# Optimization experiments

Hardware: AMD Instinct MI355X
Metric: run time of the kernel (lower is better)

Reference implementation:

```python
import jax, jax.numpy as jnp
import numpy as np

N_E = 16384
E_DIM = 256


def setup_inputs() -> dict:
    key = jax.random.key(0)
    k1, k2 = jax.random.split(key)
    z = jax.random.normal(k1, (16, E_DIM, 32, 32), dtype=jnp.float32)
    # nn.Embedding init: uniform(-1/n_e, 1/n_e)
    embedding_weight = jax.random.uniform(
        k2, (N_E, E_DIM), dtype=jnp.float32, minval=-1.0 / N_E, maxval=1.0 / N_E
    )
    return {"z": z, "embedding_weight": embedding_weight}


def reference(z, embedding_weight):
    # b c h w -> b h w c, flatten to (N, e_dim)
    zf = jnp.transpose(z, (0, 2, 3, 1)).reshape(-1, E_DIM)  # [N, d]
    # squared euclidean distances: ||z||^2 + ||e||^2 - 2 z.e^T
    d = (
        jnp.sum(zf ** 2, axis=1, keepdims=True)          # [N, 1]
        + jnp.sum(embedding_weight ** 2, axis=1)         # [n_e]
        - 2.0 * jnp.einsum("bd,nd->bn", zf, embedding_weight)  # [N, n_e]
    )
    min_encoding_indices = jnp.argmin(d, axis=1)  # [N] int
    return min_encoding_indices
```

## Files before the change

kernel.cpp:

```cpp
#include <hip/hip_runtime.h>

#define EDIM 256
#define NROW 16384
#define NCODE 16384
#define NBN 128
#define MARGIN 2.0e-4f

typedef _Float16 f16x8 __attribute__((ext_vector_type(8)));
typedef _Float16 f16x4 __attribute__((ext_vector_type(4)));
typedef float f32x4 __attribute__((ext_vector_type(4)));

__device__ __forceinline__ void gll16(const void* g, void* l) {
  __builtin_amdgcn_global_load_lds((const __attribute__((address_space(1))) void*)g,
                                   (__attribute__((address_space(3))) void*)l, 16, 0, 0);
}
__device__ __forceinline__ void gll4(const void* g, void* l) {
  __builtin_amdgcn_global_load_lds((const __attribute__((address_space(1))) void*)g,
                                   (__attribute__((address_space(3))) void*)l, 4, 0, 0);
}

__global__ __launch_bounds__(256) void k_prep_e(const float* __restrict__ e,
                                                float* __restrict__ es,
                                                _Float16* __restrict__ Eh) {
  const int row = blockIdx.x * 4 + (threadIdx.x >> 6);
  const int lane = threadIdx.x & 63;
  float4 v = *(const float4*)&e[row * EDIM + lane * 4];
  f16x4 h;
  h[0] = (_Float16)(v.x * 1024.0f);
  h[1] = (_Float16)(v.y * 1024.0f);
  h[2] = (_Float16)(v.z * 1024.0f);
  h[3] = (_Float16)(v.w * 1024.0f);
  *(f16x4*)&Eh[row * EDIM + lane * 4] = h;
  double s = (double)v.x * v.x + (double)v.y * v.y + (double)v.z * v.z + (double)v.w * v.w;
#pragma unroll
  for (int off = 32; off > 0; off >>= 1) s += __shfl_down(s, off, 64);
  if (lane == 0) es[row] = (float)s;
}

__global__ __launch_bounds__(256) void k_es(const float* __restrict__ e,
                                            float* __restrict__ es) {
  const int row = blockIdx.x * 4 + (threadIdx.x >> 6);
  const int lane = threadIdx.x & 63;
  float4 v = *(const float4*)&e[row * EDIM + lane * 4];
  double s = (double)v.x * v.x + (double)v.y * v.y + (double)v.z * v.z + (double)v.w * v.w;
#pragma unroll
  for (int off = 32; off > 0; off >>= 1) s += __shfl_down(s, off, 64);
  if (lane == 0) es[row] = (float)s;
}

__global__ __launch_bounds__(256) void k_cvt_z(const float* __restrict__ z,
                                               _Float16* __restrict__ Zh) {
  __shared__ float zl[EDIM * 33];
  const int t = threadIdx.x;
  const int rb = blockIdx.x;
  const int bb = rb >> 5;
  const int hw0 = (rb & 31) << 5;
  const float* zbase = z + (size_t)bb * EDIM * 1024 + hw0;
#pragma unroll 4
  for (int rep = 0; rep < 32; ++rep) {
    int c = rep * 8 + (t >> 5);
    zl[c * 33 + (t & 31)] = zbase[(size_t)c * 1024 + (t & 31)];
  }
  __syncthreads();
  const int mloc = t >> 3, part = t & 7;
#pragma unroll
  for (int i = 0; i < 4; ++i) {
    int c0 = part * 32 + i * 8;
    f16x8 v;
#pragma unroll
    for (int j = 0; j < 8; ++j) v[j] = (_Float16)zl[(c0 + j) * 33 + mloc];
    *(f16x8*)&Zh[(size_t)(rb * 32 + mloc) * EDIM + c0] = v;
  }
}

__global__ __launch_bounds__(256, 2) void k_gemm(const _Float16* __restrict__ Zh,
                                                 const _Float16* __restrict__ Eh,
                                                 float* __restrict__ lmin,
                                                 uint4* __restrict__ masks) {
  __shared__ __align__(16) char smem[32768];
  char* smemA = smem;
  char* smemB = smem + 16384;

  const int tid = threadIdx.x;
  const int lane = tid & 63;
  const int wv = tid >> 6;
  const int wm = wv & 1, wn = wv >> 1;
  const int fr = lane & 15;
  const int fq = lane >> 4;
  const int swz = (fq ^ ((fr >> 1) & 3)) * 16;

  const int bid = (int)blockIdx.x;
  const int wgid = (bid & 7) * 2048 + (bid >> 3);
  const int st = wgid >> 8, wi = wgid & 255;
  const int bm = ((st & 7) << 4) | (wi & 15);
  const int bn = ((st >> 3) << 4) | (wi >> 4);

  const char* zh_b = (const char*)Zh;
  const char* eh_b = (const char*)Eh;

  auto stage = [&](int buf, int s) {
#pragma unroll
    for (int i = 0; i < 2; ++i) {
      const int L = (i * 256 + tid) * 16;
      const int row = L >> 6, p = (L >> 4) & 3;
      const int gsw = (p ^ ((row >> 1) & 3)) * 16;
      gll16(zh_b + (size_t)(bm * 128 + row) * 512 + s * 64 + gsw, smemA + buf * 8192 + L);
      gll16(eh_b + (size_t)(bn * 128 + row) * 512 + s * 64 + gsw, smemB + buf * 8192 + L);
    }
  };

  f32x4 acc[4][4];
#pragma unroll
  for (int i = 0; i < 4; ++i)
#pragma unroll
    for (int j = 0; j < 4; ++j) acc[i][j] = (f32x4)0.0f;

  stage(0, 0);
  int buf = 0;
#pragma unroll 1
  for (int s = 0; s < 8; ++s) {
    if (s + 1 < 8) stage(buf ^ 1, s + 1);
    if (s + 1 < 8) {
      asm volatile("s_waitcnt vmcnt(4)\n\ts_barrier" ::: "memory");
    } else {
      asm volatile("s_waitcnt vmcnt(0)\n\ts_barrier" ::: "memory");
    }
    const char* aB = smemA + buf * 8192;
    const char* bB = smemB + buf * 8192;
    f16x8 af[4], bf[4];
#pragma unroll
    for (int mi = 0; mi < 4; ++mi)
      af[mi] = *(const f16x8*)(aB + (wm * 64 + mi * 16 + fr) * 64 + swz);
#pragma unroll
    for (int ni = 0; ni < 4; ++ni)
      bf[ni] = *(const f16x8*)(bB + (wn * 64 + ni * 16 + fr) * 64 + swz);
    __builtin_amdgcn_s_setprio(1);
#pragma unroll
    for (int mi = 0; mi < 4; ++mi)
#pragma unroll
      for (int ni = 0; ni < 4; ++ni)
        acc[mi][ni] = __builtin_amdgcn_mfma_f32_16x16x32_f16(af[mi], bf[ni], acc[mi][ni], 0, 0, 0);
    __builtin_amdgcn_s_setprio(0);
    asm volatile("s_waitcnt lgkmcnt(0)\n\ts_barrier" ::: "memory");
    buf ^= 1;
  }

  float* rowsmin = (float*)smem;
  float* rowminC = (float*)(smem + 1024);
  unsigned short* msk16 = (unsigned short*)(smem + 1536);
  const float sc = -0.001953125f;
#pragma unroll
  for (int mi = 0; mi < 4; ++mi)
#pragma unroll
    for (int r = 0; r < 4; ++r) {
      float v = acc[mi][0][r] * sc;
      v = fminf(v, acc[mi][1][r] * sc);
      v = fminf(v, acc[mi][2][r] * sc);
      v = fminf(v, acc[mi][3][r] * sc);
#pragma unroll
      for (int off = 1; off < 16; off <<= 1) v = fminf(v, __shfl_xor(v, off, 64));
      if (fr == 0) rowsmin[(wm * 64 + mi * 16 + fq * 4 + r) * 2 + wn] = v;
    }
  __syncthreads();
  if (tid < 128) {
    float rm = fminf(rowsmin[tid * 2], rowsmin[tid * 2 + 1]);
    rowminC[tid] = rm;
    lmin[(size_t)bn * NROW + bm * 128 + tid] = rm;
  }
  __syncthreads();
#pragma unroll
  for (int mi = 0; mi < 4; ++mi)
#pragma unroll
    for (int r = 0; r < 4; ++r) {
      const int row = wm * 64 + mi * 16 + fq * 4 + r;
      const float thr = rowminC[row] + MARGIN;
#pragma unroll
      for (int ni = 0; ni < 4; ++ni) {
        unsigned long long bal = __ballot(acc[mi][ni][r] * sc <= thr);
        if (fr == 0) msk16[row * 8 + wn * 4 + ni] = (unsigned short)((bal >> (fq * 16)) & 0xffffull);
      }
    }
  __syncthreads();
  if (tid < 128)
    masks[(size_t)bn * NROW + bm * 128 + tid] = *(const uint4*)&msk16[tid * 8];
}

__global__ __launch_bounds__(256) void k_rescore(const float* __restrict__ z,
                                                 const float* __restrict__ e,
                                                 const float* __restrict__ es,
                                                 const float* __restrict__ lmin,
                                                 const uint4* __restrict__ masks,
                                                 int* __restrict__ out) {
  extern __shared__ float zl[];
  float* lmin_s = zl + EDIM * 33;
  const int t = threadIdx.x;
  const int rb = (int)blockIdx.x;
  const int bb = rb >> 5;
  const int hw0 = (rb & 31) << 5;
  const int r0 = rb * 32;
  const float* zbase = z + (size_t)bb * EDIM * 1024 + hw0;
#pragma unroll 4
  for (int rep = 0; rep < 32; ++rep) {
    int c = rep * 8 + (t >> 5);
    zl[c * 33 + (t & 31)] = zbase[(size_t)c * 1024 + (t & 31)];
  }
#pragma unroll 4
  for (int rep = 0; rep < 16; ++rep) {
    int bn = rep * 8 + (t >> 5);
    lmin_s[bn * 33 + (t & 31)] = lmin[(size_t)bn * NROW + r0 + (t & 31)];
  }
  __syncthreads();

  const int r = t >> 3, q8 = t & 7, q = q8 & 3;
  const int row = r0 + r;

  double sq = 0.0;
  {
    const float* zq = zl + (q * 64) * 33 + r;
    for (int k = 0; k < 64; ++k) {
      float v = zq[k * 33];
      sq = fma((double)v, (double)v, sq);
    }
  }
  double s01 = sq + __shfl_xor(sq, 1, 64);
  double zsd = s01 + __shfl_xor(s01, 2, 64);
  const float zs = (float)zsd;

  float g = 3.402823466e+38f;
#pragma unroll
  for (int j = 0; j < 16; ++j) g = fminf(g, lmin_s[(q8 * 16 + j) * 33 + r]);
  g = fminf(g, __shfl_xor(g, 1, 64));
  g = fminf(g, __shfl_xor(g, 2, 64));
  g = fminf(g, __shfl_xor(g, 4, 64));
  const float thr = g + MARGIN;

  float bestd = 3.402823466e+38f;
  int besti = 0x7fffffff;
#pragma unroll 1
  for (int j = 0; j < 16; ++j) {
    const int bn = q8 * 16 + j;
    if (lmin_s[bn * 33 + r] <= thr) {
      uint4 mk = masks[(size_t)bn * NROW + row];
      unsigned w[4] = {mk.x, mk.y, mk.z, mk.w};
#pragma unroll 1
      for (int qq = 0; qq < 4; ++qq) {
        unsigned u = w[qq];
        while (u) {
          int b = __ffs(u) - 1;
          u &= u - 1;
          const int code = bn * 128 + qq * 32 + b;
          const float* ep = e + (size_t)code * EDIM;
          float dot = 0.0f;
          for (int k = 0; k < EDIM; k += 4) {
            float4 ev = *(const float4*)(ep + k);
            dot = fmaf(zl[(k + 0) * 33 + r], ev.x, dot);
            dot = fmaf(zl[(k + 1) * 33 + r], ev.y, dot);
            dot = fmaf(zl[(k + 2) * 33 + r], ev.z, dot);
            dot = fmaf(zl[(k + 3) * 33 + r], ev.w, dot);
          }
          float d = (zs + es[code]) - 2.0f * dot;
          if (d < bestd) {
            bestd = d;
            besti = code;
          }
        }
      }
    }
  }
#pragma unroll
  for (int off = 1; off <= 4; off <<= 1) {
    float ov = __shfl_xor(bestd, off, 64);
    int oi = __shfl_xor(besti, off, 64);
    if (ov < bestd || (ov == bestd && oi < besti)) {
      bestd = ov;
      besti = oi;
    }
  }
  if (q8 == 0) out[row] = besti;
}

__global__ __launch_bounds__(256) void k_merge(const float* __restrict__ candv,
                                               const int* __restrict__ candi,
                                               int* __restrict__ out) {
  int n = blockIdx.x * 256 + threadIdx.x;
  float v0 = candv[n], v1 = candv[NROW + n];
  int i0 = candi[n], i1 = candi[NROW + n];
  out[n] = (v1 < v0) ? i1 : i0;
}

template <int SPLIT>
__global__ __launch_bounds__(256, 2) void k_main_fb(const float* __restrict__ z,
                                                    const float* __restrict__ e,
                                                    const float* __restrict__ es,
                                                    float* __restrict__ candv,
                                                    int* __restrict__ candi,
                                                    int* __restrict__ outd) {
  extern __shared__ char smemc[];
  float* As = (float*)smemc;
  float* Bs = (float*)(smemc + 16384);
  double* zred = (double*)(smemc + 16384 + 32768);
  float* zsf = (float*)(smemc + 16384 + 32768 + 2048);
  const int tid = threadIdx.x;
  const int lane = tid & 63;
  const int wv = tid >> 6;
  const int tm = tid & 7;
  const int tn = tid >> 3;
  const int rt = (int)blockIdx.x / SPLIT;
  const int sp = (int)blockIdx.x % SPLIT;
  const int bb = rt >> 4;
  const int hw0 = (rt & 15) << 6;
  const float* zb = z + bb * (EDIM * 1024) + hw0;
  const int codeBase = sp * (NCODE / SPLIT);
  const int NSTEP = (NCODE / SPLIT) / 256 * 8;
  auto stageA = [&](int buf, int gts) {
    const int k0 = (gts & 7) * 32;
    const float* g0 = zb + (size_t)k0 * 1024 + lane;
    float* l0 = As + buf * 2048 + (wv * 8) * 64;
#pragma unroll
    for (int s = 0; s < 8; ++s) gll4(g0 + (size_t)(wv * 8 + s) * 1024, l0 + s * 64);
  };
  float4 bpre[8];
  auto loadB = [&](int gts) {
    const int ct = gts >> 3, k0 = (gts & 7) * 32;
    const float* g = e + (size_t)(codeBase + ct * 256 + tid) * 256 + k0;
#pragma unroll
    for (int s = 0; s < 8; ++s) bpre[s] = *(const float4*)(g + s * 4);
  };
  auto writeB = [&](int buf) {
    float* bw_ = Bs + buf * 8192 + tid;
#pragma unroll
    for (int s = 0; s < 8; ++s) {
      bw_[(4 * s + 0) * 256] = bpre[s].x;
      bw_[(4 * s + 1) * 256] = bpre[s].y;
      bw_[(4 * s + 2) * 256] = bpre[s].z;
      bw_[(4 * s + 3) * 256] = bpre[s].w;
    }
  };
  stageA(0, 0);
  loadB(0);
  {
    const int m = tid & 63, qt = tid >> 6;
    const float* zp = zb + (size_t)(qt * 64) * 1024 + m;
    double s = 0.0;
    for (int k = 0; k < 64; ++k) {
      float v = zp[(size_t)k * 1024];
      s = fma((double)v, (double)v, s);
    }
    zred[qt * 64 + m] = s;
  }
  writeB(0);
  __syncthreads();
  if (tid < 64) {
    double sz = (zred[tid] + zred[64 + tid]) + (zred[128 + tid] + zred[192 + tid]);
    zsf[tid] = (float)sz;
  }
  __syncthreads();
  float zsr[8];
#pragma unroll
  for (int i = 0; i < 8; ++i) zsr[i] = zsf[tm * 8 + i];
  __syncthreads();
  float bestv[8];
  int besti[8];
#pragma unroll
  for (int i = 0; i < 8; ++i) {
    bestv[i] = 3.402823466e+38f;
    besti[i] = 0;
  }
  float acc[8][8];
  int cur = 0;
#pragma unroll 1
  for (int step = 0; step < NSTEP; ++step) {
    const int kc = step & 7, ct = step >> 3;
    if (step + 1 < NSTEP) {
      stageA(cur ^ 1, step + 1);
      loadB(step + 1);
    }
    if (kc == 0) {
#pragma unroll
      for (int i = 0; i < 8; ++i)
#pragma unroll
        for (int j = 0; j < 8; ++j) acc[i][j] = 0.0f;
    }
    const float* ak = As + cur * 2048 + tm * 8;
    const float* bk = Bs + cur * 8192 + tn * 8;
#pragma unroll 4
    for (int k = 0; k < 32; ++k) {
      float4 a0 = *(const float4*)(ak + k * 64);
      float4 a1 = *(const float4*)(ak + k * 64 + 4);
      float4 b0 = *(const float4*)(bk + k * 256);
      float4 b1 = *(const float4*)(bk + k * 256 + 4);
      float av[8] = {a0.x, a0.y, a0.z, a0.w, a1.x, a1.y, a1.z, a1.w};
      float bw[8] = {b0.x, b0.y, b0.z, b0.w, b1.x, b1.y, b1.z, b1.w};
#pragma unroll
      for (int i = 0; i < 8; ++i)
#pragma unroll
        for (int j = 0; j < 8; ++j) acc[i][j] = fmaf(av[i], bw[j], acc[i][j]);
    }
    if (step + 1 < NSTEP) writeB(cur ^ 1);
    if (kc == 7) {
      const int cb = codeBase + ct * 256 + tn * 8;
#pragma unroll
      for (int j = 0; j < 8; ++j) {
        float ej = es[cb + j];
#pragma unroll
        for (int i = 0; i < 8; ++i) {
          float d = (zsr[i] + ej) - 2.0f * acc[i][j];
          if (d < bestv[i]) {
            bestv[i] = d;
            besti[i] = cb + j;
          }
        }
      }
    }
    __syncthreads();
    cur ^= 1;
  }
  float* Lv = (float*)(smemc + 16384);
  int* Li = (int*)(smemc + 16384 + 8192);
#pragma unroll
  for (int i = 0; i < 8; ++i) {
    Lv[(tm * 8 + i) * 32 + tn] = bestv[i];
    Li[(tm * 8 + i) * 32 + tn] = besti[i];
  }
  __syncthreads();
  if (tid < 64) {
    float bv = Lv[tid * 32];
    int bi = Li[tid * 32];
#pragma unroll 1
    for (int g2 = 1; g2 < 32; ++g2) {
      float v = Lv[tid * 32 + g2];
      int ii = Li[tid * 32 + g2];
      if (v < bv || (v == bv && ii < bi)) {
        bv = v;
        bi = ii;
      }
    }
    if (SPLIT == 1) outd[rt * 64 + tid] = bi;
    else {
      candv[sp * NROW + rt * 64 + tid] = bv;
      candi[sp * NROW + rt * 64 + tid] = bi;
    }
  }
}

extern "C" void kernel_launch(void* const* d_in, const int* in_sizes, int n_in,
                              void* d_out, int out_size, void* d_ws, size_t ws_size,
                              hipStream_t stream) {
  const float* z = (const float*)d_in[0];
  const float* e = (const float*)d_in[1];
  int* out = (int*)d_out;

  char* ws = (char*)d_ws;
  float* es = (float*)ws;
  const size_t off_zh = 65536;
  const size_t off_eh = off_zh + (size_t)NROW * EDIM * 2;
  const size_t off_lmin = off_eh + (size_t)NCODE * EDIM * 2;
  const size_t off_masks = off_lmin + (size_t)NROW * NBN * 4;
  const size_t need = off_masks + (size_t)NROW * NBN * 16;

  if (ws_size >= need) {
    _Float16* Zh = (_Float16*)(ws + off_zh);
    _Float16* Eh = (_Float16*)(ws + off_eh);
    float* lmin = (float*)(ws + off_lmin);
    uint4* masks = (uint4*)(ws + off_masks);
    k_prep_e<<<dim3(NCODE / 4), dim3(256), 0, stream>>>(e, es, Eh);
    k_cvt_z<<<dim3(512), dim3(256), 0, stream>>>(z, Zh);
    k_gemm<<<dim3(16384), dim3(256), 0, stream>>>(Zh, Eh, lmin, masks);
    const int rs_smem = (EDIM * 33 + NBN * 33) * 4;
    hipFuncSetAttribute(reinterpret_cast<const void*>(&k_rescore),
                        hipFuncAttributeMaxDynamicSharedMemorySize, rs_smem);
    k_rescore<<<dim3(512), dim3(256), rs_smem, stream>>>(z, e, es, lmin, masks, out);
  } else {
    k_es<<<dim3(NCODE / 4), dim3(256), 0, stream>>>(e, es);
    float* candv = (float*)(ws + 65536);
    int* candi = (int*)(ws + 65536 + 131072);
    const size_t smem = 16384 + 65536;
    if (ws_size >= 65536 + 131072 + 131072) {
      hipFuncSetAttribute(reinterpret_cast<const void*>(&k_main_fb<2>),
                          hipFuncAttributeMaxDynamicSharedMemorySize, (int)smem);
      k_main_fb<2><<<dim3(512), dim3(256), smem, stream>>>(z, e, es, candv, candi, out);
      k_merge<<<dim3(NROW / 256), dim3(256), 0, stream>>>(candv, candi, out);
    } else {
      hipFuncSetAttribute(reinterpret_cast<const void*>(&k_main_fb<1>),
                          hipFuncAttributeMaxDynamicSharedMemorySize, (int)smem);
      k_main_fb<1><<<dim3(256), dim3(256), smem, stream>>>(z, e, es, candv, candi, out);
    }
  }
}
```

Measured before the change: 348.0 us.

## Use 8 waves per GEMM block with 64x32 wave tiles and max-based threshold

Raises the GEMM workgroup from 4 to 8 waves. Each wave now computes a 64x32 tile instead of 64x64, and each thread issues one global-to-LDS load per operand per stage instead of two. The per-row min is now taken as a max over raw dot products, and the mask compare is done against a precomputed threshold in raw units, which removes the per-element scaling. The intent is more latency hiding and fewer accumulator registers per wave. The cost is more barrier participants, a smaller MFMA-to-LDS-read ratio per wave, and launch bounds of 8 blocks per CU that may force register spills.

```diff
diff --git a/kernel.cpp b/kernel.cpp
--- a/kernel.cpp
+++ b/kernel.cpp
@@ -73,7 +73,7 @@
   }
 }
 
-__global__ __launch_bounds__(256, 2) void k_gemm(const _Float16* __restrict__ Zh,
+__global__ __launch_bounds__(512, 8) void k_gemm(const _Float16* __restrict__ Zh,
                                                  const _Float16* __restrict__ Eh,
                                                  float* __restrict__ lmin,
                                                  uint4* __restrict__ masks) {
@@ -84,7 +84,8 @@
   const int tid = threadIdx.x;
   const int lane = tid & 63;
   const int wv = tid >> 6;
-  const int wm = wv & 1, wn = wv >> 1;
+  const int wm = wv & 1;
+  const int wn = wv >> 1;
   const int fr = lane & 15;
   const int fq = lane >> 4;
   const int swz = (fq ^ ((fr >> 1) & 3)) * 16;
@@ -98,73 +99,69 @@
   const char* zh_b = (const char*)Zh;
   const char* eh_b = (const char*)Eh;
 
+  const int L = tid * 16;
+  const int srow = L >> 6, sp_ = (L >> 4) & 3;
+  const int gsw = (sp_ ^ ((srow >> 1) & 3)) * 16;
   auto stage = [&](int buf, int s) {
-#pragma unroll
-    for (int i = 0; i < 2; ++i) {
-      const int L = (i * 256 + tid) * 16;
-      const int row = L >> 6, p = (L >> 4) & 3;
-      const int gsw = (p ^ ((row >> 1) & 3)) * 16;
-      gll16(zh_b + (size_t)(bm * 128 + row) * 512 + s * 64 + gsw, smemA + buf * 8192 + L);
-      gll16(eh_b + (size_t)(bn * 128 + row) * 512 + s * 64 + gsw, smemB + buf * 8192 + L);
-    }
+    gll16(zh_b + (size_t)(bm * 128 + srow) * 512 + s * 64 + gsw, smemA + buf * 8192 + L);
+    gll16(eh_b + (size_t)(bn * 128 + srow) * 512 + s * 64 + gsw, smemB + buf * 8192 + L);
   };
 
-  f32x4 acc[4][4];
+  f32x4 acc[4][2];
 #pragma unroll
   for (int i = 0; i < 4; ++i)
 #pragma unroll
-    for (int j = 0; j < 4; ++j) acc[i][j] = (f32x4)0.0f;
+    for (int j = 0; j < 2; ++j) acc[i][j] = (f32x4)0.0f;
 
   stage(0, 0);
   int buf = 0;
 #pragma unroll 1
   for (int s = 0; s < 8; ++s) {
-    if (s + 1 < 8) stage(buf ^ 1, s + 1);
     if (s + 1 < 8) {
-      asm volatile("s_waitcnt vmcnt(4)\n\ts_barrier" ::: "memory");
+      stage(buf ^ 1, s + 1);
+      asm volatile("s_waitcnt vmcnt(2)\n\ts_barrier" ::: "memory");
     } else {
       asm volatile("s_waitcnt vmcnt(0)\n\ts_barrier" ::: "memory");
     }
     const char* aB = smemA + buf * 8192;
     const char* bB = smemB + buf * 8192;
-    f16x8 af[4], bf[4];
+    f16x8 af[4], bf[2];
 #pragma unroll
     for (int mi = 0; mi < 4; ++mi)
       af[mi] = *(const f16x8*)(aB + (wm * 64 + mi * 16 + fr) * 64 + swz);
 #pragma unroll
-    for (int ni = 0; ni < 4; ++ni)
-      bf[ni] = *(const f16x8*)(bB + (wn * 64 + ni * 16 + fr) * 64 + swz);
+    for (int ni = 0; ni < 2; ++ni)
+      bf[ni] = *(const f16x8*)(bB + (wn * 32 + ni * 16 + fr) * 64 + swz);
     __builtin_amdgcn_s_setprio(1);
 #pragma unroll
     for (int mi = 0; mi < 4; ++mi)
 #pragma unroll
-      for (int ni = 0; ni < 4; ++ni)
+      for (int ni = 0; ni < 2; ++ni)
         acc[mi][ni] = __builtin_amdgcn_mfma_f32_16x16x32_f16(af[mi], bf[ni], acc[mi][ni], 0, 0, 0);
     __builtin_amdgcn_s_setprio(0);
     asm volatile("s_waitcnt lgkmcnt(0)\n\ts_barrier" ::: "memory");
     buf ^= 1;
   }
 
-  float* rowsmin = (float*)smem;
-  float* rowminC = (float*)(smem + 1024);
-  unsigned short* msk16 = (unsigned short*)(smem + 1536);
+  float* rowsmax = (float*)smem;
+  float* thrs = (float*)(smem + 2048);
+  unsigned short* msk16 = (unsigned short*)(smem + 2560);
   const float sc = -0.001953125f;
 #pragma unroll
   for (int mi = 0; mi < 4; ++mi)
 #pragma unroll
     for (int r = 0; r < 4; ++r) {
-      float v = acc[mi][0][r] * sc;
-      v = fminf(v, acc[mi][1][r] * sc);
-      v = fminf(v, acc[mi][2][r] * sc);
-      v = fminf(v, acc[mi][3][r] * sc);
-#pragma unroll
-      for (int off = 1; off < 16; off <<= 1) v = fminf(v, __shfl_xor(v, off, 64));
-      if (fr == 0) rowsmin[(wm * 64 + mi * 16 + fq * 4 + r) * 2 + wn] = v;
+      float v = fmaxf(acc[mi][0][r], acc[mi][1][r]);
+#pragma unroll
+      for (int off = 1; off < 16; off <<= 1) v = fmaxf(v, __shfl_xor(v, off, 64));
+      if (fr == 0) rowsmax[(wm * 64 + mi * 16 + fq * 4 + r) * 4 + wn] = v;
     }
   __syncthreads();
   if (tid < 128) {
-    float rm = fminf(rowsmin[tid * 2], rowsmin[tid * 2 + 1]);
-    rowminC[tid] = rm;
+    float mx = fmaxf(fmaxf(rowsmax[tid * 4], rowsmax[tid * 4 + 1]),
+                     fmaxf(rowsmax[tid * 4 + 2], rowsmax[tid * 4 + 3]));
+    float rm = sc * mx;
+    thrs[tid] = (rm + MARGIN) * (-512.0f);
     lmin[(size_t)bn * NROW + bm * 128 + tid] = rm;
   }
   __syncthreads();
@@ -173,11 +170,12 @@
 #pragma unroll
     for (int r = 0; r < 4; ++r) {
       const int row = wm * 64 + mi * 16 + fq * 4 + r;
-      const float thr = rowminC[row] + MARGIN;
-#pragma unroll
-      for (int ni = 0; ni < 4; ++ni) {
-        unsigned long long bal = __ballot(acc[mi][ni][r] * sc <= thr);
-        if (fr == 0) msk16[row * 8 + wn * 4 + ni] = (unsigned short)((bal >> (fq * 16)) & 0xffffull);
+      const float th = thrs[row];
+#pragma unroll
+      for (int ni = 0; ni < 2; ++ni) {
+        unsigned long long bal = __ballot(acc[mi][ni][r] >= th);
+        if (fr == 0)
+          msk16[row * 8 + wn * 2 + ni] = (unsigned short)((bal >> (fq * 16)) & 0xffffull);
       }
     }
   __syncthreads();
@@ -465,7 +463,7 @@
     uint4* masks = (uint4*)(ws + off_masks);
     k_prep_e<<<dim3(NCODE / 4), dim3(256), 0, stream>>>(e, es, Eh);
     k_cvt_z<<<dim3(512), dim3(256), 0, stream>>>(z, Zh);
-    k_gemm<<<dim3(16384), dim3(256), 0, stream>>>(Zh, Eh, lmin, masks);
+    k_gemm<<<dim3(16384), dim3(512), 0, stream>>>(Zh, Eh, lmin, masks);
     const int rs_smem = (EDIM * 33 + NBN * 33) * 4;
     hipFuncSetAttribute(reinterpret_cast<const void*>(&k_rescore),
                         hipFuncAttributeMaxDynamicSharedMemorySize, rs_smem);
```

Result: slower. 387.6 us (+11.4%).
